# Optimization experiments

Measured on AMD Instinct MI355X. Metric: run time of the kernel, lower is better.

## Reference

```python
import jax, jax.numpy as jnp
import numpy as np

N_CLASSES = 3
FEAT_SIZES = (64, 32)  # source1 64x64, source2 32x32 for 512x512 input


def conv(x, w, b):
    # x: NCHW, w: OIHW, 3x3 SAME, stride 1
    y = jax.lax.conv_general_dilated(
        x, w, window_strides=(1, 1), padding='SAME',
        dimension_numbers=('NCHW', 'OIHW', 'NCHW'))
    return y + b[None, :, None, None]


def maxpool(x):
    return jax.lax.reduce_window(x, -jnp.inf, jax.lax.max,
                                 (1, 1, 2, 2), (1, 1, 2, 2), 'VALID')


def l2norm(x, gamma, eps=1e-10):
    # standard SSD L2Norm: per-position channel L2 normalize, learned per-channel scale
    n = jnp.sqrt(jnp.sum(x * x, axis=1, keepdims=True)) + eps
    return gamma[None, :, None, None] * x / n


def make_priors():
    # PriorBox: one prior per feature-map cell, normalized (cx, cy) centers
    ps = []
    for f in FEAT_SIZES:
        c = (jnp.arange(f, dtype=jnp.float32) + 0.5) / f
        cy, cx = jnp.meshgrid(c, c, indexing='ij')
        ps.append(jnp.stack([cx.ravel(), cy.ravel()], axis=1))  # [f*f, 2]
    return jnp.concatenate(ps, axis=0)  # [5120, 2]


def setup_inputs() -> dict:
    key = jax.random.key(0)
    ks = iter(jax.random.split(key, 32))

    def he(k, shape):
        fan_in = shape[1] * shape[2] * shape[3]
        return jax.random.normal(k, shape, jnp.float32) * (2.0 / fan_in) ** 0.5

    d = {'x': jax.random.normal(next(ks), (8, 2, 512, 512), jnp.float32)}
    shapes = [(64, 2, 3, 3), (64, 64, 3, 3), (128, 64, 3, 3), (128, 128, 3, 3),
              (256, 128, 3, 3), (256, 256, 3, 3), (256, 256, 3, 3), (256, 256, 3, 3)]
    for n, s in enumerate(shapes, 1):
        d[f'w{n}'] = he(next(ks), s)
        d[f'b{n}'] = jnp.zeros((s[0],), jnp.float32)
    d['g1'] = 20.0 * jnp.ones((256,), jnp.float32)  # L2Norm1 weight
    d['g2'] = 20.0 * jnp.ones((256,), jnp.float32)  # L2Norm2 weight
    for pre, oc in (('l', 2), ('c', N_CLASSES), ('r', 1)):
        for si in (1, 2):
            d[f'{pre}w{si}'] = he(next(ks), (oc, 256, 3, 3))
            d[f'{pre}b{si}'] = jnp.zeros((oc,), jnp.float32)
    return d


def reference(x, w1, b1, w2, b2, w3, b3, w4, b4, w5, b5, w6, b6, w7, b7, w8, b8,
              g1, g2, lw1, lb1, lw2, lb2, cw1, cb1, cw2, cb2, rw1, rb1, rw2, rb2):
    B = x.shape[0]
    r = jax.nn.relu
    # vgg[0:33]
    x = r(conv(x, w1, b1)); x = r(conv(x, w2, b2)); x = maxpool(x)
    x = r(conv(x, w3, b3)); x = r(conv(x, w4, b4)); x = maxpool(x)
    x = r(conv(x, w5, b5)); x = r(conv(x, w6, b6)); x = maxpool(x)
    s1 = l2norm(x, g1)                 # [B,256,64,64]
    # vgg[33:]
    x = maxpool(x)
    x = r(conv(x, w7, b7)); x = r(conv(x, w8, b8))
    s2 = l2norm(x, g2)                 # [B,256,32,32]

    def head(s, w_, b_):
        # conv -> permute(0,2,3,1) -> flatten, as in the torch forward
        return conv(s, w_, b_).transpose(0, 2, 3, 1).reshape(B, -1)

    loc = jnp.concatenate([head(s1, lw1, lb1), head(s2, lw2, lb2)], 1).reshape(B, -1, 2)
    conf = jnp.concatenate([head(s1, cw1, cb1), head(s2, cw2, cb2)], 1).reshape(B, -1, N_CLASSES)
    regr = jnp.concatenate([head(s1, rw1, rb1), head(s2, rw2, rb2)], 1).reshape(B, -1, 1)
    priors = make_priors()
    return loc, conf, regr, priors
```

## Files before the change

kernel.cpp:

```cpp
#include <hip/hip_runtime.h>

typedef _Float16 f16;
typedef _Float16 f16x8 __attribute__((ext_vector_type(8)));
typedef float f32x4 __attribute__((ext_vector_type(4)));

__device__ __forceinline__ f32x4 mfma16(f16x8 a, f16x8 b, f32x4 c) {
    return __builtin_amdgcn_mfma_f32_16x16x32_f16(a, b, c, 0, 0, 0);
}

template<int IC, int OC, int BX, int WY, int WO, int MT, bool POOL>
__global__ __launch_bounds__(256) void convmf_k(
    const f16* __restrict__ in, const f16* __restrict__ wt,
    const float* __restrict__ bias, f16* __restrict__ out,
    int H, int W, int ocBlocks, long inStride, long outStride)
{
    constexpr int WROWS = MT * 16 / BX;
    constexpr int BROWS = WROWS * WY;
    constexpr int SR = BROWS + 2;
    constexpr int SC = BX + 2;
    constexpr int LOG = (BX == 64) ? 6 : 5;
    static_assert(!POOL || (BX == 64 && MT == 8), "pool path assumes BX==64, MT==8");
    __shared__ f16 lds[SR * SC * 40];

    const int tid  = threadIdx.x;
    const int lane = tid & 63;
    const int wv   = tid >> 6;
    const int wy   = wv / WO;
    const int wo   = wv % WO;
    const int lm   = lane & 15;
    const int lk   = lane >> 4;
    const int x0   = blockIdx.x * BX;
    const int y0   = blockIdx.y * BROWS;
    const int zb   = blockIdx.z;
    const int n    = zb / ocBlocks;
    const int oc0  = (zb - n * ocBlocks) * (64 * WO) + wo * 64;
    in  += (long)n * inStride;
    out += (long)n * outStride;

    f32x4 acc[MT][4];
#pragma unroll
    for (int mt = 0; mt < MT; ++mt)
#pragma unroll
        for (int nt = 0; nt < 4; ++nt)
            acc[mt][nt] = (f32x4){0.f, 0.f, 0.f, 0.f};

    const int Wp = W + 2;
    for (int ic0 = 0; ic0 < IC; ic0 += 32) {
        if (ic0) __syncthreads();
        const f16* ip = in + ((long)y0 * Wp + x0) * IC + ic0;
        constexpr int TASKS = SR * SC * 4;
        for (int s = tid; s < TASKS; s += 256) {
            int r    = s / (SC * 4);
            int rem  = s - r * (SC * 4);
            int xcol = rem >> 2;
            int g    = rem & 3;
            f16x8 v = *(const f16x8*)(ip + ((long)r * Wp + xcol) * IC + g * 8);
            *(f16x8*)&lds[(r * SC + xcol) * 40 + g * 8] = v;
        }
        __syncthreads();

        for (int t = 0; t < 9; ++t) {
            int dy = t / 3, dx = t - dy * 3;
            const f16* wp = wt + ((long)t * OC + oc0) * IC + ic0 + lk * 8;
            f16x8 b0 = *(const f16x8*)(wp + (0 * 16 + lm) * IC);
            f16x8 b1 = *(const f16x8*)(wp + (1 * 16 + lm) * IC);
            f16x8 b2 = *(const f16x8*)(wp + (2 * 16 + lm) * IC);
            f16x8 b3 = *(const f16x8*)(wp + (3 * 16 + lm) * IC);
#pragma unroll
            for (int mt = 0; mt < MT; ++mt) {
                int pos = mt * 16 + lm;
                int xx = pos & (BX - 1);
                int yy = wy * WROWS + (pos >> LOG);
                f16x8 a = *(const f16x8*)&lds[((yy + dy) * SC + xx + dx) * 40 + lk * 8];
                acc[mt][0] = mfma16(a, b0, acc[mt][0]);
                acc[mt][1] = mfma16(a, b1, acc[mt][1]);
                acc[mt][2] = mfma16(a, b2, acc[mt][2]);
                acc[mt][3] = mfma16(a, b3, acc[mt][3]);
            }
        }
    }

    if constexpr (!POOL) {
#pragma unroll
        for (int nt = 0; nt < 4; ++nt) {
            int oc = oc0 + nt * 16 + lm;
            float bs = bias[oc];
#pragma unroll
            for (int mt = 0; mt < MT; ++mt) {
#pragma unroll
                for (int r = 0; r < 4; ++r) {
                    int pos = mt * 16 + lk * 4 + r;
                    int xx = pos & (BX - 1);
                    int yy = wy * WROWS + (pos >> LOG);
                    float v = fmaxf(acc[mt][nt][r] + bs, 0.f);
                    out[((long)(y0 + yy + 1) * (W + 2) + (x0 + xx + 1)) * OC + oc] = (f16)v;
                }
            }
        }
    } else {
        const int Wo = W >> 1;
#pragma unroll
        for (int nt = 0; nt < 4; ++nt) {
            int oc = oc0 + nt * 16 + lm;
            float bs = bias[oc];
#pragma unroll
            for (int mt = 0; mt < 4; ++mt) {
#pragma unroll
                for (int r = 0; r < 4; r += 2) {
                    float v = fmaxf(fmaxf(acc[mt][nt][r], acc[mt][nt][r + 1]),
                                    fmaxf(acc[mt + 4][nt][r], acc[mt + 4][nt][r + 1]));
                    v = fmaxf(v + bs, 0.f);
                    int pos = mt * 16 + lk * 4 + r;
                    int xo = pos >> 1;
                    out[((long)((y0 >> 1) + wy + 1) * (Wo + 2) + ((x0 >> 1) + xo + 1)) * OC + oc] = (f16)v;
                }
            }
        }
    }
}

__global__ __launch_bounds__(256) void conv12_k(
    const float* __restrict__ x,
    const f16* __restrict__ wt1,
    const float* __restrict__ b1,
    const f16* __restrict__ wt2,
    const float* __restrict__ b2,
    f16* __restrict__ p1, int itemBase, long outStride)
{
    __shared__ f16 ldsx[12 * 68 * 2];
    __shared__ f16 a1t[10 * 66 * 40];
    const int tid = threadIdx.x;
    const int lane = tid & 63;
    const int wv = tid >> 6;
    const int lm = lane & 15;
    const int lk = lane >> 4;
    const int x0 = blockIdx.x * 64;
    const int y0 = blockIdx.y * 8;
    const float* xb = x + (long)(itemBase + blockIdx.z) * 2 * 512 * 512;
    f16* out = p1 + (long)blockIdx.z * outStride;

    for (int s = tid; s < 12 * 68 * 2; s += 256) {
        int ch = s & 1;
        int v = s >> 1;
        int r = v / 68, c = v - r * 68;
        int gy = y0 + r - 2, gx = x0 + c - 2;
        f16 val = (f16)0.f;
        if ((unsigned)gy < 512u && (unsigned)gx < 512u)
            val = (f16)xb[((long)ch * 512 + gy) * 512 + gx];
        ldsx[s] = val;
    }
    __syncthreads();

    f32x4 acc[8][4];
#pragma unroll
    for (int mt = 0; mt < 8; ++mt)
#pragma unroll
        for (int nt = 0; nt < 4; ++nt)
            acc[mt][nt] = (f32x4){0.f, 0.f, 0.f, 0.f};

    for (int cc = 0; cc < 2; ++cc) {
        if (cc) __syncthreads();

        {
            float bs0 = b1[cc * 32 + lm];
            float bs1 = b1[cc * 32 + 16 + lm];
            f16x8 bf0 = *(const f16x8*)(wt1 + (cc * 32 + lm) * 32 + lk * 8);
            f16x8 bf1 = *(const f16x8*)(wt1 + (cc * 32 + 16 + lm) * 32 + lk * 8);
            const int t0 = wv * 11;
            const int tn = (wv == 3) ? 9 : 11;
            for (int ti = 0; ti < tn; ++ti) {
                const int tile = t0 + ti;
                const int pixA = tile * 16 + lm;
                int rA = (pixA * 993) >> 16;
                int cA = pixA - rA * 66;
                f16x8 af;
#pragma unroll
                for (int j = 0; j < 8; ++j) {
                    int k = lk * 8 + j;
                    f16 v = (f16)0.f;
                    if (k < 18) {
                        int t = k >> 1, ic = k & 1;
                        int dy = (t * 22) >> 6;
                        int dx = t - 3 * dy;
                        v = ldsx[((rA + dy) * 68 + (cA + dx)) * 2 + ic];
                    }
                    af[j] = v;
                }
                f32x4 c0 = (f32x4){0.f, 0.f, 0.f, 0.f};
                f32x4 c1 = (f32x4){0.f, 0.f, 0.f, 0.f};
                c0 = mfma16(af, bf0, c0);
                c1 = mfma16(af, bf1, c1);
#pragma unroll
                for (int rr = 0; rr < 4; ++rr) {
                    int pix = tile * 16 + lk * 4 + rr;
                    if (pix < 660) {
                        int rP = (pix * 993) >> 16;
                        int cP = pix - rP * 66;
                        bool valid = ((unsigned)(y0 + rP - 1) < 512u) &&
                                     ((unsigned)(x0 + cP - 1) < 512u);
                        float v0 = valid ? fmaxf(c0[rr] + bs0, 0.f) : 0.f;
                        float v1 = valid ? fmaxf(c1[rr] + bs1, 0.f) : 0.f;
                        a1t[pix * 40 + lm] = (f16)v0;
                        a1t[pix * 40 + 16 + lm] = (f16)v1;
                    }
                }
            }
        }
        __syncthreads();

        const int ic0 = cc * 32;
        for (int t = 0; t < 9; ++t) {
            int dy = t / 3, dx = t - dy * 3;
            const f16* wp = wt2 + ((long)t * 64) * 64 + ic0 + lk * 8;
            f16x8 b0 = *(const f16x8*)(wp + (0 * 16 + lm) * 64);
            f16x8 bb1 = *(const f16x8*)(wp + (1 * 16 + lm) * 64);
            f16x8 b2v = *(const f16x8*)(wp + (2 * 16 + lm) * 64);
            f16x8 b3 = *(const f16x8*)(wp + (3 * 16 + lm) * 64);
#pragma unroll
            for (int mt = 0; mt < 8; ++mt) {
                int pos = mt * 16 + lm;
                int xx = pos & 63;
                int yy = wv * 2 + (pos >> 6);
                f16x8 a = *(const f16x8*)&a1t[((yy + dy) * 66 + xx + dx) * 40 + lk * 8];
                acc[mt][0] = mfma16(a, b0, acc[mt][0]);
                acc[mt][1] = mfma16(a, bb1, acc[mt][1]);
                acc[mt][2] = mfma16(a, b2v, acc[mt][2]);
                acc[mt][3] = mfma16(a, b3, acc[mt][3]);
            }
        }
    }

#pragma unroll
    for (int nt = 0; nt < 4; ++nt) {
        int oc = nt * 16 + lm;
        float bs = b2[oc];
#pragma unroll
        for (int mt = 0; mt < 4; ++mt) {
#pragma unroll
            for (int r = 0; r < 4; r += 2) {
                float v = fmaxf(fmaxf(acc[mt][nt][r], acc[mt][nt][r + 1]),
                                fmaxf(acc[mt + 4][nt][r], acc[mt + 4][nt][r + 1]));
                v = fmaxf(v + bs, 0.f);
                int pos = mt * 16 + lk * 4 + r;
                int xo = pos >> 1;
                out[((long)((y0 >> 1) + wv + 1) * 258 + ((x0 >> 1) + xo + 1)) * 64 + oc] = (f16)v;
            }
        }
    }
}

template<int BX>
__global__ __launch_bounds__(256) void headconv_k(
    const f16* __restrict__ s, long sStride, const f16* __restrict__ wth,
    const float* __restrict__ lb, const float* __restrict__ cb, const float* __restrict__ rb,
    float* __restrict__ loc, float* __restrict__ conf, float* __restrict__ regr,
    int W, int posoff)
{
    constexpr int BY = (BX == 64) ? 1 : 2;
    constexpr int SR = BY + 2, SC = BX + 2;
    constexpr int LOG = (BX == 64) ? 6 : 5;
    __shared__ f16 lds[SR * SC * 40];
    const int tid = threadIdx.x;
    const int lane = tid & 63;
    const int wv = tid >> 6;
    const int lm = lane & 15;
    const int lk = lane >> 4;
    const int y0 = blockIdx.y * BY;
    const int b = blockIdx.z;
    s += (long)b * sStride;

    f32x4 acc = (f32x4){0.f, 0.f, 0.f, 0.f};
    const int Wp = W + 2;
    for (int ic0 = 0; ic0 < 256; ic0 += 32) {
        if (ic0) __syncthreads();
        const f16* ip = s + (long)y0 * Wp * 256 + ic0;
        constexpr int TASKS = SR * SC * 4;
        for (int t = tid; t < TASKS; t += 256) {
            int r = t / (SC * 4);
            int rem = t - r * (SC * 4);
            int xcol = rem >> 2, g = rem & 3;
            f16x8 v = *(const f16x8*)(ip + ((long)r * Wp + xcol) * 256 + g * 8);
            *(f16x8*)&lds[(r * SC + xcol) * 40 + g * 8] = v;
        }
        __syncthreads();
        for (int t = 0; t < 9; ++t) {
            int dy = t / 3, dx = t - dy * 3;
            f16x8 bf = *(const f16x8*)(wth + ((long)t * 16 + lm) * 256 + ic0 + lk * 8);
            int pos = wv * 16 + lm;
            int xx = pos & (BX - 1), yy = pos >> LOG;
            f16x8 a = *(const f16x8*)&lds[((yy + dy) * SC + xx + dx) * 40 + lk * 8];
            acc = mfma16(a, bf, acc);
        }
    }
#pragma unroll
    for (int r = 0; r < 4; ++r) {
        int pos = wv * 16 + lk * 4 + r;
        int xx = pos & (BX - 1), yy = pos >> LOG;
        int P = posoff + (y0 + yy) * W + xx;
        float v = acc[r];
        if (lm < 2)       loc[((long)b * 5120 + P) * 2 + lm]       = v + lb[lm];
        else if (lm < 5)  conf[((long)b * 5120 + P) * 3 + (lm - 2)] = v + cb[lm - 2];
        else if (lm == 5) regr[(long)b * 5120 + P]                  = v + rb[0];
    }
}

__global__ __launch_bounds__(256) void cvt_wt_k(const float* __restrict__ w, f16* __restrict__ wt,
                                                int OC, int IC)
{
    int idx = blockIdx.x * 256 + threadIdx.x;
    if (idx >= OC * IC) return;
    int oc = idx / IC, ic = idx - oc * IC;
#pragma unroll
    for (int t = 0; t < 9; ++t)
        wt[((long)t * OC + oc) * IC + ic] = (f16)w[(long)idx * 9 + t];
}

__global__ __launch_bounds__(64) void cvt_wt1_k(const float* __restrict__ w, f16* __restrict__ wt1)
{
    int oc = threadIdx.x;
#pragma unroll
    for (int k = 0; k < 32; ++k) {
        f16 v = (f16)0.f;
        if (k < 18) {
            int t = k >> 1, ic = k & 1;
            v = (f16)w[((long)oc * 2 + ic) * 9 + t];
        }
        wt1[oc * 32 + k] = v;
    }
}

__global__ __launch_bounds__(256) void cvt_wth_k(const float* __restrict__ lw, const float* __restrict__ cw,
                                                 const float* __restrict__ rw, f16* __restrict__ wth)
{
    int idx = blockIdx.x * 256 + threadIdx.x;
    if (idx >= 9 * 16 * 256) return;
    int t = idx / (16 * 256);
    int r = (idx / 256) & 15;
    int ic = idx & 255;
    float v = 0.f;
    if (r < 2)      v = lw[((long)r * 256 + ic) * 9 + t];
    else if (r < 5) v = cw[((long)(r - 2) * 256 + ic) * 9 + t];
    else if (r == 5) v = rw[(long)ic * 9 + t];
    wth[((long)t * 16 + r) * 256 + ic] = (f16)v;
}

__global__ __launch_bounds__(256) void halo_k(f16* __restrict__ buf, int W, int H, int C,
                                              long stride, int items)
{
    int per = (2 * (W + 2) + 2 * H) * C;
    long total = (long)per * items;
    long idx = (long)blockIdx.x * 256 + threadIdx.x;
    if (idx >= total) return;
    int n = idx / per;
    int j = idx - (long)n * per;
    int c = j % C, p = j / C;
    int row, col;
    if (p < W + 2) { row = 0; col = p; }
    else if (p < 2 * (W + 2)) { row = H + 1; col = p - (W + 2); }
    else { int q = p - 2 * (W + 2); row = 1 + (q >> 1); col = (q & 1) ? (W + 1) : 0; }
    buf[(long)n * stride + ((long)row * (W + 2) + col) * C + c] = (f16)0.f;
}

__global__ __launch_bounds__(256) void l2n_k(const f16* __restrict__ in, const float* __restrict__ g,
                                             f16* __restrict__ out, int W, long stride, int total)
{
    int i = blockIdx.x * 256 + threadIdx.x;
    if (i >= total) return;
    int b = i / (W * W);
    int rem = i - b * W * W;
    int y = rem / W, x = rem - y * W;
    long off = (long)b * stride + ((long)(y + 1) * (W + 2) + x + 1) * 256;
    const f16* p = in + off;
    f16* q = out + off;
    float s = 0.f;
    for (int gg = 0; gg < 32; ++gg) {
        f16x8 v = *(const f16x8*)(p + gg * 8);
#pragma unroll
        for (int j = 0; j < 8; ++j) { float f = (float)v[j]; s = fmaf(f, f, s); }
    }
    float inv = 1.f / (sqrtf(s) + 1e-10f);
    for (int gg = 0; gg < 32; ++gg) {
        f16x8 v = *(const f16x8*)(p + gg * 8);
        f16x8 o;
#pragma unroll
        for (int j = 0; j < 8; ++j) o[j] = (f16)(g[gg * 8 + j] * ((float)v[j] * inv));
        *(f16x8*)(q + gg * 8) = o;
    }
}

__global__ __launch_bounds__(256) void mp_k(const f16* __restrict__ in, f16* __restrict__ out)
{
    int idx = blockIdx.x * 256 + threadIdx.x;
    if (idx >= 8 * 32 * 32 * 32) return;
    int gg = idx & 31;
    int xo = (idx >> 5) & 31;
    int yo = (idx >> 10) & 31;
    int b = idx >> 15;
    const f16* p = in + (long)b * 1115136 + ((long)(2 * yo + 1) * 66 + 2 * xo + 1) * 256 + gg * 8;
    f16x8 a0 = *(const f16x8*)p;
    f16x8 a1 = *(const f16x8*)(p + 256);
    f16x8 a2 = *(const f16x8*)(p + 66 * 256);
    f16x8 a3 = *(const f16x8*)(p + 66 * 256 + 256);
    f16x8 o;
#pragma unroll
    for (int j = 0; j < 8; ++j)
        o[j] = (f16)fmaxf(fmaxf((float)a0[j], (float)a1[j]), fmaxf((float)a2[j], (float)a3[j]));
    *(f16x8*)(out + (long)b * 295936 + ((long)(yo + 1) * 34 + xo + 1) * 256 + gg * 8) = o;
}

__global__ __launch_bounds__(256) void priors_k(float* __restrict__ out)
{
    int r = blockIdx.x * 256 + threadIdx.x;
    if (r >= 5120) return;
    float cx, cy;
    if (r < 4096) {
        int i = r >> 6, j = r & 63;
        cx = (j + 0.5f) / 64.0f; cy = (i + 0.5f) / 64.0f;
    } else {
        int rr = r - 4096;
        int i = rr >> 5, j = rr & 31;
        cx = (j + 0.5f) / 32.0f; cy = (i + 0.5f) / 32.0f;
    }
    out[2 * r] = cx;
    out[2 * r + 1] = cy;
}

extern "C" void kernel_launch(void* const* d_in, const int* in_sizes, int n_in,
                              void* d_out, int out_size, void* d_ws, size_t ws_size,
                              hipStream_t stream)
{
    const float* x  = (const float*)d_in[0];
    const float* w1 = (const float*)d_in[1];  const float* b1 = (const float*)d_in[2];
    const float* w2 = (const float*)d_in[3];  const float* b2 = (const float*)d_in[4];
    const float* w3 = (const float*)d_in[5];  const float* b3 = (const float*)d_in[6];
    const float* w4 = (const float*)d_in[7];  const float* b4 = (const float*)d_in[8];
    const float* w5 = (const float*)d_in[9];  const float* b5 = (const float*)d_in[10];
    const float* w6 = (const float*)d_in[11]; const float* b6 = (const float*)d_in[12];
    const float* w7 = (const float*)d_in[13]; const float* b7 = (const float*)d_in[14];
    const float* w8 = (const float*)d_in[15]; const float* b8 = (const float*)d_in[16];
    const float* g1 = (const float*)d_in[17]; const float* g2 = (const float*)d_in[18];
    const float* lw1 = (const float*)d_in[19]; const float* lb1 = (const float*)d_in[20];
    const float* lw2 = (const float*)d_in[21]; const float* lb2 = (const float*)d_in[22];
    const float* cw1 = (const float*)d_in[23]; const float* cb1 = (const float*)d_in[24];
    const float* cw2 = (const float*)d_in[25]; const float* cb2 = (const float*)d_in[26];
    const float* rw1 = (const float*)d_in[27]; const float* rb1 = (const float*)d_in[28];
    const float* rw2 = (const float*)d_in[29]; const float* rb2 = (const float*)d_in[30];

    f16* wsh = (f16*)d_ws;
    f16* wt2  = wsh + 0;
    f16* wt3  = wsh + 36864;
    f16* wt4  = wsh + 110592;
    f16* wt5  = wsh + 258048;
    f16* wt6  = wsh + 552960;
    f16* wt7  = wsh + 1142784;
    f16* wt8  = wsh + 1732608;
    f16* wt1  = wsh + 2322432;
    f16* wth1 = wsh + 2324480;
    f16* wth2 = wsh + 2361344;
    f16* x6p  = wsh + 2398208;
    const long PI = 11319296;

    const long R1S = 4260096;
    const long PS  = 12780288;
    const long PH2 = 18391040;

    int G = 1;
    for (int g = 8; g >= 1; g >>= 1) {
        long ext = (long)g * PS; if (ext < PH2) ext = PH2;
        if (2.0 * (double)(PI + ext) <= (double)ws_size) { G = g; break; }
    }
    const int NGRP = 8 / G;

    f16* p1 = wsh + PI;
    f16* a3 = wsh + PI + R1S;
    f16* p2 = p1;
    f16* a5 = a3;
    f16* s1 = wsh + PI;
    f16* p4 = wsh + PI + 8921088;
    f16* a7 = wsh + PI + 11288576;
    f16* a8 = wsh + PI + 13656064;
    f16* s2 = wsh + PI + 16023552;

    float* loc  = (float*)d_out;
    float* conf = loc + 81920;
    float* regr = loc + 204800;
    float* pri  = loc + 245760;

    cvt_wt_k<<<dim3((64 * 64 + 255) / 256), 256, 0, stream>>>(w2, wt2, 64, 64);
    cvt_wt_k<<<dim3((128 * 64 + 255) / 256), 256, 0, stream>>>(w3, wt3, 128, 64);
    cvt_wt_k<<<dim3((128 * 128 + 255) / 256), 256, 0, stream>>>(w4, wt4, 128, 128);
    cvt_wt_k<<<dim3((256 * 128 + 255) / 256), 256, 0, stream>>>(w5, wt5, 256, 128);
    cvt_wt_k<<<dim3((256 * 256 + 255) / 256), 256, 0, stream>>>(w6, wt6, 256, 256);
    cvt_wt_k<<<dim3((256 * 256 + 255) / 256), 256, 0, stream>>>(w7, wt7, 256, 256);
    cvt_wt_k<<<dim3((256 * 256 + 255) / 256), 256, 0, stream>>>(w8, wt8, 256, 256);
    cvt_wt1_k<<<dim3(1), 64, 0, stream>>>(w1, wt1);
    cvt_wth_k<<<dim3(144), 256, 0, stream>>>(lw1, cw1, rw1, wth1);
    cvt_wth_k<<<dim3(144), 256, 0, stream>>>(lw2, cw2, rw2, wth2);

    for (int grp = 0; grp < NGRP; ++grp) {
        f16* x6g = x6p + (long)grp * G * 1115136;
        halo_k<<<dim3((G * (2 * 258 + 2 * 256) * 64 + 255) / 256), 256, 0, stream>>>(p1, 256, 256, 64, PS, G);
        halo_k<<<dim3((G * (2 * 258 + 2 * 256) * 128 + 255) / 256), 256, 0, stream>>>(a3, 256, 256, 128, PS, G);
        conv12_k<<<dim3(8, 64, G), 256, 0, stream>>>(x, wt1, b1, wt2, b2, p1, grp * G, PS);
        convmf_k<64, 128, 64, 2, 2, 8, false><<<dim3(4, 64, G), 256, 0, stream>>>(
            p1, wt3, b3, a3, 256, 256, 1, PS, PS);
        halo_k<<<dim3((G * (2 * 130 + 2 * 128) * 128 + 255) / 256), 256, 0, stream>>>(p2, 128, 128, 128, PS, G);
        convmf_k<128, 128, 64, 2, 2, 8, true><<<dim3(4, 64, G), 256, 0, stream>>>(
            a3, wt4, b4, p2, 256, 256, 1, PS, PS);
        halo_k<<<dim3((G * (2 * 130 + 2 * 128) * 256 + 255) / 256), 256, 0, stream>>>(a5, 128, 128, 256, PS, G);
        convmf_k<128, 256, 64, 2, 2, 8, false><<<dim3(2, 32, 2 * G), 256, 0, stream>>>(
            p2, wt5, b5, a5, 128, 128, 2, PS, PS);
        convmf_k<256, 256, 64, 2, 2, 8, true><<<dim3(2, 32, 2 * G), 256, 0, stream>>>(
            a5, wt6, b6, x6g, 128, 128, 2, PS, 1115136);
    }

    halo_k<<<dim3((8 * (2 * 66 + 2 * 64) * 256 + 255) / 256), 256, 0, stream>>>(s1, 64, 64, 256, 1115136, 8);
    halo_k<<<dim3((8 * (2 * 34 + 2 * 32) * 256 + 255) / 256), 256, 0, stream>>>(p4, 32, 32, 256, 295936, 8);
    halo_k<<<dim3((8 * (2 * 34 + 2 * 32) * 256 + 255) / 256), 256, 0, stream>>>(a7, 32, 32, 256, 295936, 8);
    halo_k<<<dim3((8 * (2 * 34 + 2 * 32) * 256 + 255) / 256), 256, 0, stream>>>(s2, 32, 32, 256, 295936, 8);

    l2n_k<<<dim3((32768 + 255) / 256), 256, 0, stream>>>(x6p, g1, s1, 64, 1115136, 32768);
    mp_k<<<dim3((262144 + 255) / 256), 256, 0, stream>>>(x6p, p4);
    convmf_k<256, 256, 32, 2, 2, 4, false><<<dim3(1, 8, 16), 256, 0, stream>>>(
        p4, wt7, b7, a7, 32, 32, 2, 295936, 295936);
    convmf_k<256, 256, 32, 2, 2, 4, false><<<dim3(1, 8, 16), 256, 0, stream>>>(
        a7, wt8, b8, a8, 32, 32, 2, 295936, 295936);
    l2n_k<<<dim3((8192 + 255) / 256), 256, 0, stream>>>(a8, g2, s2, 32, 295936, 8192);

    headconv_k<64><<<dim3(1, 64, 8), 256, 0, stream>>>(
        s1, 1115136, wth1, lb1, cb1, rb1, loc, conf, regr, 64, 0);
    headconv_k<32><<<dim3(1, 16, 8), 256, 0, stream>>>(
        s2, 295936, wth2, lb2, cb2, rb2, loc, conf, regr, 32, 4096);
    priors_k<<<dim3(20), 256, 0, stream>>>(pri);

    (void)in_sizes; (void)n_in; (void)out_size; (void)ws_size;
}
```

Measured before the change: 1.351 ms.

## Halve per-wave output-channel tile and raise occupancy in conv kernels

Adds an NT template parameter so each wave computes 32 output channels instead of 64 in the large-resolution conv layers, doubling the grid's oc-block count, and sets launch_bounds(256,4) to target more resident blocks. conv12_k is also restructured to a 4-row tile with waves split over rows and output channels, shrinking LDS and accumulator registers. The aim is higher occupancy and better latency hiding, but each input tile is now loaded and reused across fewer output channels, which raises LDS fill and global input traffic.

```diff
diff --git a/kernel.cpp b/kernel.cpp
--- a/kernel.cpp
+++ b/kernel.cpp
@@ -8,8 +8,8 @@
     return __builtin_amdgcn_mfma_f32_16x16x32_f16(a, b, c, 0, 0, 0);
 }
 
-template<int IC, int OC, int BX, int WY, int WO, int MT, bool POOL>
-__global__ __launch_bounds__(256) void convmf_k(
+template<int IC, int OC, int BX, int WY, int WO, int MT, int NT, bool POOL>
+__global__ __launch_bounds__(256, 4) void convmf_k(
     const f16* __restrict__ in, const f16* __restrict__ wt,
     const float* __restrict__ bias, f16* __restrict__ out,
     int H, int W, int ocBlocks, long inStride, long outStride)
@@ -33,15 +33,15 @@
     const int y0   = blockIdx.y * BROWS;
     const int zb   = blockIdx.z;
     const int n    = zb / ocBlocks;
-    const int oc0  = (zb - n * ocBlocks) * (64 * WO) + wo * 64;
+    const int oc0  = (zb - n * ocBlocks) * (16 * NT * WO) + wo * (16 * NT);
     in  += (long)n * inStride;
     out += (long)n * outStride;
 
-    f32x4 acc[MT][4];
+    f32x4 acc[MT][NT];
 #pragma unroll
     for (int mt = 0; mt < MT; ++mt)
 #pragma unroll
-        for (int nt = 0; nt < 4; ++nt)
+        for (int nt = 0; nt < NT; ++nt)
             acc[mt][nt] = (f32x4){0.f, 0.f, 0.f, 0.f};
 
     const int Wp = W + 2;
@@ -62,27 +62,26 @@
         for (int t = 0; t < 9; ++t) {
             int dy = t / 3, dx = t - dy * 3;
             const f16* wp = wt + ((long)t * OC + oc0) * IC + ic0 + lk * 8;
-            f16x8 b0 = *(const f16x8*)(wp + (0 * 16 + lm) * IC);
-            f16x8 b1 = *(const f16x8*)(wp + (1 * 16 + lm) * IC);
-            f16x8 b2 = *(const f16x8*)(wp + (2 * 16 + lm) * IC);
-            f16x8 b3 = *(const f16x8*)(wp + (3 * 16 + lm) * IC);
+            f16x8 bfr[NT];
+#pragma unroll
+            for (int nt = 0; nt < NT; ++nt)
+                bfr[nt] = *(const f16x8*)(wp + (nt * 16 + lm) * IC);
 #pragma unroll
             for (int mt = 0; mt < MT; ++mt) {
                 int pos = mt * 16 + lm;
                 int xx = pos & (BX - 1);
                 int yy = wy * WROWS + (pos >> LOG);
                 f16x8 a = *(const f16x8*)&lds[((yy + dy) * SC + xx + dx) * 40 + lk * 8];
-                acc[mt][0] = mfma16(a, b0, acc[mt][0]);
-                acc[mt][1] = mfma16(a, b1, acc[mt][1]);
-                acc[mt][2] = mfma16(a, b2, acc[mt][2]);
-                acc[mt][3] = mfma16(a, b3, acc[mt][3]);
+#pragma unroll
+                for (int nt = 0; nt < NT; ++nt)
+                    acc[mt][nt] = mfma16(a, bfr[nt], acc[mt][nt]);
             }
         }
     }
 
     if constexpr (!POOL) {
 #pragma unroll
-        for (int nt = 0; nt < 4; ++nt) {
+        for (int nt = 0; nt < NT; ++nt) {
             int oc = oc0 + nt * 16 + lm;
             float bs = bias[oc];
 #pragma unroll
@@ -100,7 +99,7 @@
     } else {
         const int Wo = W >> 1;
 #pragma unroll
-        for (int nt = 0; nt < 4; ++nt) {
+        for (int nt = 0; nt < NT; ++nt) {
             int oc = oc0 + nt * 16 + lm;
             float bs = bias[oc];
 #pragma unroll
@@ -119,7 +118,7 @@
     }
 }
 
-__global__ __launch_bounds__(256) void conv12_k(
+__global__ __launch_bounds__(256, 4) void conv12_k(
     const float* __restrict__ x,
     const f16* __restrict__ wt1,
     const float* __restrict__ b1,
@@ -127,19 +126,21 @@
     const float* __restrict__ b2,
     f16* __restrict__ p1, int itemBase, long outStride)
 {
-    __shared__ f16 ldsx[12 * 68 * 2];
-    __shared__ f16 a1t[10 * 66 * 40];
+    __shared__ f16 ldsx[8 * 68 * 2];
+    __shared__ f16 a1t[6 * 66 * 40];
     const int tid = threadIdx.x;
     const int lane = tid & 63;
     const int wv = tid >> 6;
+    const int wy = wv >> 1;
+    const int wo = wv & 1;
     const int lm = lane & 15;
     const int lk = lane >> 4;
     const int x0 = blockIdx.x * 64;
-    const int y0 = blockIdx.y * 8;
+    const int y0 = blockIdx.y * 4;
     const float* xb = x + (long)(itemBase + blockIdx.z) * 2 * 512 * 512;
     f16* out = p1 + (long)blockIdx.z * outStride;
 
-    for (int s = tid; s < 12 * 68 * 2; s += 256) {
+    for (int s = tid; s < 8 * 68 * 2; s += 256) {
         int ch = s & 1;
         int v = s >> 1;
         int r = v / 68, c = v - r * 68;
@@ -151,11 +152,11 @@
     }
     __syncthreads();
 
-    f32x4 acc[8][4];
+    f32x4 acc[8][2];
 #pragma unroll
     for (int mt = 0; mt < 8; ++mt)
 #pragma unroll
-        for (int nt = 0; nt < 4; ++nt)
+        for (int nt = 0; nt < 2; ++nt)
             acc[mt][nt] = (f32x4){0.f, 0.f, 0.f, 0.f};
 
     for (int cc = 0; cc < 2; ++cc) {
@@ -166,13 +167,11 @@
             float bs1 = b1[cc * 32 + 16 + lm];
             f16x8 bf0 = *(const f16x8*)(wt1 + (cc * 32 + lm) * 32 + lk * 8);
             f16x8 bf1 = *(const f16x8*)(wt1 + (cc * 32 + 16 + lm) * 32 + lk * 8);
-            const int t0 = wv * 11;
-            const int tn = (wv == 3) ? 9 : 11;
-            for (int ti = 0; ti < tn; ++ti) {
-                const int tile = t0 + ti;
+            for (int tile = wv; tile < 25; tile += 4) {
                 const int pixA = tile * 16 + lm;
-                int rA = (pixA * 993) >> 16;
-                int cA = pixA - rA * 66;
+                const int pixg = (pixA < 396) ? pixA : 0;
+                int rA = (pixg * 993) >> 16;
+                int cA = pixg - rA * 66;
                 f16x8 af;
 #pragma unroll
                 for (int j = 0; j < 8; ++j) {
@@ -193,7 +192,7 @@
 #pragma unroll
                 for (int rr = 0; rr < 4; ++rr) {
                     int pix = tile * 16 + lk * 4 + rr;
-                    if (pix < 660) {
+                    if (pix < 396) {
                         int rP = (pix * 993) >> 16;
                         int cP = pix - rP * 66;
                         bool valid = ((unsigned)(y0 + rP - 1) < 512u) &&
@@ -211,28 +210,24 @@
         const int ic0 = cc * 32;
         for (int t = 0; t < 9; ++t) {
             int dy = t / 3, dx = t - dy * 3;
-            const f16* wp = wt2 + ((long)t * 64) * 64 + ic0 + lk * 8;
-            f16x8 b0 = *(const f16x8*)(wp + (0 * 16 + lm) * 64);
+            const f16* wp = wt2 + ((long)t * 64 + wo * 32) * 64 + ic0 + lk * 8;
+            f16x8 bb0 = *(const f16x8*)(wp + (0 * 16 + lm) * 64);
             f16x8 bb1 = *(const f16x8*)(wp + (1 * 16 + lm) * 64);
-            f16x8 b2v = *(const f16x8*)(wp + (2 * 16 + lm) * 64);
-            f16x8 b3 = *(const f16x8*)(wp + (3 * 16 + lm) * 64);
 #pragma unroll
             for (int mt = 0; mt < 8; ++mt) {
                 int pos = mt * 16 + lm;
                 int xx = pos & 63;
-                int yy = wv * 2 + (pos >> 6);
+                int yy = wy * 2 + (pos >> 6);
                 f16x8 a = *(const f16x8*)&a1t[((yy + dy) * 66 + xx + dx) * 40 + lk * 8];
-                acc[mt][0] = mfma16(a, b0, acc[mt][0]);
+                acc[mt][0] = mfma16(a, bb0, acc[mt][0]);
                 acc[mt][1] = mfma16(a, bb1, acc[mt][1]);
-                acc[mt][2] = mfma16(a, b2v, acc[mt][2]);
-                acc[mt][3] = mfma16(a, b3, acc[mt][3]);
             }
         }
     }
 
 #pragma unroll
-    for (int nt = 0; nt < 4; ++nt) {
-        int oc = nt * 16 + lm;
+    for (int nt = 0; nt < 2; ++nt) {
+        int oc = wo * 32 + nt * 16 + lm;
         float bs = b2[oc];
 #pragma unroll
         for (int mt = 0; mt < 4; ++mt) {
@@ -243,7 +238,7 @@
                 v = fmaxf(v + bs, 0.f);
                 int pos = mt * 16 + lk * 4 + r;
                 int xo = pos >> 1;
-                out[((long)((y0 >> 1) + wv + 1) * 258 + ((x0 >> 1) + xo + 1)) * 64 + oc] = (f16)v;
+                out[((long)((y0 >> 1) + wy + 1) * 258 + ((x0 >> 1) + xo + 1)) * 64 + oc] = (f16)v;
             }
         }
     }
@@ -501,17 +496,17 @@
         f16* x6g = x6p + (long)grp * G * 1115136;
         halo_k<<<dim3((G * (2 * 258 + 2 * 256) * 64 + 255) / 256), 256, 0, stream>>>(p1, 256, 256, 64, PS, G);
         halo_k<<<dim3((G * (2 * 258 + 2 * 256) * 128 + 255) / 256), 256, 0, stream>>>(a3, 256, 256, 128, PS, G);
-        conv12_k<<<dim3(8, 64, G), 256, 0, stream>>>(x, wt1, b1, wt2, b2, p1, grp * G, PS);
-        convmf_k<64, 128, 64, 2, 2, 8, false><<<dim3(4, 64, G), 256, 0, stream>>>(
-            p1, wt3, b3, a3, 256, 256, 1, PS, PS);
+        conv12_k<<<dim3(8, 128, G), 256, 0, stream>>>(x, wt1, b1, wt2, b2, p1, grp * G, PS);
+        convmf_k<64, 128, 64, 2, 2, 8, 2, false><<<dim3(4, 64, 2 * G), 256, 0, stream>>>(
+            p1, wt3, b3, a3, 256, 256, 2, PS, PS);
         halo_k<<<dim3((G * (2 * 130 + 2 * 128) * 128 + 255) / 256), 256, 0, stream>>>(p2, 128, 128, 128, PS, G);
-        convmf_k<128, 128, 64, 2, 2, 8, true><<<dim3(4, 64, G), 256, 0, stream>>>(
-            a3, wt4, b4, p2, 256, 256, 1, PS, PS);
+        convmf_k<128, 128, 64, 2, 2, 8, 2, true><<<dim3(4, 64, 2 * G), 256, 0, stream>>>(
+            a3, wt4, b4, p2, 256, 256, 2, PS, PS);
         halo_k<<<dim3((G * (2 * 130 + 2 * 128) * 256 + 255) / 256), 256, 0, stream>>>(a5, 128, 128, 256, PS, G);
-        convmf_k<128, 256, 64, 2, 2, 8, false><<<dim3(2, 32, 2 * G), 256, 0, stream>>>(
-            p2, wt5, b5, a5, 128, 128, 2, PS, PS);
-        convmf_k<256, 256, 64, 2, 2, 8, true><<<dim3(2, 32, 2 * G), 256, 0, stream>>>(
-            a5, wt6, b6, x6g, 128, 128, 2, PS, 1115136);
+        convmf_k<128, 256, 64, 2, 2, 8, 2, false><<<dim3(2, 32, 4 * G), 256, 0, stream>>>(
+            p2, wt5, b5, a5, 128, 128, 4, PS, PS);
+        convmf_k<256, 256, 64, 2, 2, 8, 2, true><<<dim3(2, 32, 4 * G), 256, 0, stream>>>(
+            a5, wt6, b6, x6g, 128, 128, 4, PS, 1115136);
     }
 
     halo_k<<<dim3((8 * (2 * 66 + 2 * 64) * 256 + 255) / 256), 256, 0, stream>>>(s1, 64, 64, 256, 1115136, 8);
@@ -521,9 +516,9 @@
 
     l2n_k<<<dim3((32768 + 255) / 256), 256, 0, stream>>>(x6p, g1, s1, 64, 1115136, 32768);
     mp_k<<<dim3((262144 + 255) / 256), 256, 0, stream>>>(x6p, p4);
-    convmf_k<256, 256, 32, 2, 2, 4, false><<<dim3(1, 8, 16), 256, 0, stream>>>(
+    convmf_k<256, 256, 32, 2, 2, 4, 4, false><<<dim3(1, 8, 16), 256, 0, stream>>>(
         p4, wt7, b7, a7, 32, 32, 2, 295936, 295936);
-    convmf_k<256, 256, 32, 2, 2, 4, false><<<dim3(1, 8, 16), 256, 0, stream>>>(
+    convmf_k<256, 256, 32, 2, 2, 4, 4, false><<<dim3(1, 8, 16), 256, 0, stream>>>(
         a7, wt8, b8, a8, 32, 32, 2, 295936, 295936);
     l2n_k<<<dim3((8192 + 255) / 256), 256, 0, stream>>>(a8, g2, s2, 32, 295936, 8192);
 
```

After: 2.228 ms. 64.9% more time.

## Halve conv12 block height and split output channels across wave pairs

Applied to the files above, without the earlier changes.

The fused conv1+conv2+pool kernel now handles 4 input rows per block instead of 8. Waves are arranged 2x2, with each pair splitting the 64 output channels. This cuts LDS use (smaller ldsx and a1t tiles) and accumulator registers per thread, which should allow more blocks per CU and doubles the grid. The conv1 A-fragment gather now reads both input channels with one 32-bit LDS load instead of per-element 16-bit loads. In exchange, the halo recompute ratio for conv1 rises, since each block recomputes 6 rows of conv1 for 4 output rows.

```diff
diff --git a/kernel.cpp b/kernel.cpp
--- a/kernel.cpp
+++ b/kernel.cpp
@@ -127,19 +127,21 @@
     const float* __restrict__ b2,
     f16* __restrict__ p1, int itemBase, long outStride)
 {
-    __shared__ f16 ldsx[12 * 68 * 2];
-    __shared__ f16 a1t[10 * 66 * 40];
+    __shared__ f16 ldsx[8 * 68 * 2];
+    __shared__ f16 a1t[6 * 66 * 40];
     const int tid = threadIdx.x;
     const int lane = tid & 63;
     const int wv = tid >> 6;
+    const int wy = wv >> 1;
+    const int wo = wv & 1;
     const int lm = lane & 15;
     const int lk = lane >> 4;
     const int x0 = blockIdx.x * 64;
-    const int y0 = blockIdx.y * 8;
+    const int y0 = blockIdx.y * 4;
     const float* xb = x + (long)(itemBase + blockIdx.z) * 2 * 512 * 512;
     f16* out = p1 + (long)blockIdx.z * outStride;
 
-    for (int s = tid; s < 12 * 68 * 2; s += 256) {
+    for (int s = tid; s < 8 * 68 * 2; s += 256) {
         int ch = s & 1;
         int v = s >> 1;
         int r = v / 68, c = v - r * 68;
@@ -151,11 +153,11 @@
     }
     __syncthreads();
 
-    f32x4 acc[8][4];
+    f32x4 acc[8][2];
 #pragma unroll
     for (int mt = 0; mt < 8; ++mt)
 #pragma unroll
-        for (int nt = 0; nt < 4; ++nt)
+        for (int nt = 0; nt < 2; ++nt)
             acc[mt][nt] = (f32x4){0.f, 0.f, 0.f, 0.f};
 
     for (int cc = 0; cc < 2; ++cc) {
@@ -166,34 +168,31 @@
             float bs1 = b1[cc * 32 + 16 + lm];
             f16x8 bf0 = *(const f16x8*)(wt1 + (cc * 32 + lm) * 32 + lk * 8);
             f16x8 bf1 = *(const f16x8*)(wt1 + (cc * 32 + 16 + lm) * 32 + lk * 8);
-            const int t0 = wv * 11;
-            const int tn = (wv == 3) ? 9 : 11;
-            for (int ti = 0; ti < tn; ++ti) {
-                const int tile = t0 + ti;
+            for (int tile = wv; tile < 25; tile += 4) {
                 const int pixA = tile * 16 + lm;
-                int rA = (pixA * 993) >> 16;
-                int cA = pixA - rA * 66;
-                f16x8 af;
-#pragma unroll
-                for (int j = 0; j < 8; ++j) {
-                    int k = lk * 8 + j;
-                    f16 v = (f16)0.f;
-                    if (k < 18) {
-                        int t = k >> 1, ic = k & 1;
+                const int pixg = (pixA < 396) ? pixA : 0;
+                int rA = (pixg * 993) >> 16;
+                int cA = pixg - rA * 66;
+                union { f16x8 v; unsigned u[4]; } af;
+#pragma unroll
+                for (int jj = 0; jj < 4; ++jj) {
+                    int t = lk * 4 + jj;
+                    unsigned uv = 0u;
+                    if (t < 9) {
                         int dy = (t * 22) >> 6;
                         int dx = t - 3 * dy;
-                        v = ldsx[((rA + dy) * 68 + (cA + dx)) * 2 + ic];
+                        uv = *(const unsigned*)&ldsx[((rA + dy) * 68 + (cA + dx)) * 2];
                     }
-                    af[j] = v;
+                    af.u[jj] = uv;
                 }
                 f32x4 c0 = (f32x4){0.f, 0.f, 0.f, 0.f};
                 f32x4 c1 = (f32x4){0.f, 0.f, 0.f, 0.f};
-                c0 = mfma16(af, bf0, c0);
-                c1 = mfma16(af, bf1, c1);
+                c0 = mfma16(af.v, bf0, c0);
+                c1 = mfma16(af.v, bf1, c1);
 #pragma unroll
                 for (int rr = 0; rr < 4; ++rr) {
                     int pix = tile * 16 + lk * 4 + rr;
-                    if (pix < 660) {
+                    if (pix < 396) {
                         int rP = (pix * 993) >> 16;
                         int cP = pix - rP * 66;
                         bool valid = ((unsigned)(y0 + rP - 1) < 512u) &&
@@ -211,28 +210,24 @@
         const int ic0 = cc * 32;
         for (int t = 0; t < 9; ++t) {
             int dy = t / 3, dx = t - dy * 3;
-            const f16* wp = wt2 + ((long)t * 64) * 64 + ic0 + lk * 8;
-            f16x8 b0 = *(const f16x8*)(wp + (0 * 16 + lm) * 64);
+            const f16* wp = wt2 + ((long)t * 64 + wo * 32) * 64 + ic0 + lk * 8;
+            f16x8 bb0 = *(const f16x8*)(wp + (0 * 16 + lm) * 64);
             f16x8 bb1 = *(const f16x8*)(wp + (1 * 16 + lm) * 64);
-            f16x8 b2v = *(const f16x8*)(wp + (2 * 16 + lm) * 64);
-            f16x8 b3 = *(const f16x8*)(wp + (3 * 16 + lm) * 64);
 #pragma unroll
             for (int mt = 0; mt < 8; ++mt) {
                 int pos = mt * 16 + lm;
                 int xx = pos & 63;
-                int yy = wv * 2 + (pos >> 6);
+                int yy = wy * 2 + (pos >> 6);
                 f16x8 a = *(const f16x8*)&a1t[((yy + dy) * 66 + xx + dx) * 40 + lk * 8];
-                acc[mt][0] = mfma16(a, b0, acc[mt][0]);
+                acc[mt][0] = mfma16(a, bb0, acc[mt][0]);
                 acc[mt][1] = mfma16(a, bb1, acc[mt][1]);
-                acc[mt][2] = mfma16(a, b2v, acc[mt][2]);
-                acc[mt][3] = mfma16(a, b3, acc[mt][3]);
             }
         }
     }
 
 #pragma unroll
-    for (int nt = 0; nt < 4; ++nt) {
-        int oc = nt * 16 + lm;
+    for (int nt = 0; nt < 2; ++nt) {
+        int oc = wo * 32 + nt * 16 + lm;
         float bs = b2[oc];
 #pragma unroll
         for (int mt = 0; mt < 4; ++mt) {
@@ -243,7 +238,7 @@
                 v = fmaxf(v + bs, 0.f);
                 int pos = mt * 16 + lk * 4 + r;
                 int xo = pos >> 1;
-                out[((long)((y0 >> 1) + wv + 1) * 258 + ((x0 >> 1) + xo + 1)) * 64 + oc] = (f16)v;
+                out[((long)((y0 >> 1) + wy + 1) * 258 + ((x0 >> 1) + xo + 1)) * 64 + oc] = (f16)v;
             }
         }
     }
@@ -501,7 +496,7 @@
         f16* x6g = x6p + (long)grp * G * 1115136;
         halo_k<<<dim3((G * (2 * 258 + 2 * 256) * 64 + 255) / 256), 256, 0, stream>>>(p1, 256, 256, 64, PS, G);
         halo_k<<<dim3((G * (2 * 258 + 2 * 256) * 128 + 255) / 256), 256, 0, stream>>>(a3, 256, 256, 128, PS, G);
-        conv12_k<<<dim3(8, 64, G), 256, 0, stream>>>(x, wt1, b1, wt2, b2, p1, grp * G, PS);
+        conv12_k<<<dim3(8, 128, G), 256, 0, stream>>>(x, wt1, b1, wt2, b2, p1, grp * G, PS);
         convmf_k<64, 128, 64, 2, 2, 8, false><<<dim3(4, 64, G), 256, 0, stream>>>(
             p1, wt3, b3, a3, 256, 256, 1, PS, PS);
         halo_k<<<dim3((G * (2 * 130 + 2 * 128) * 128 + 255) / 256), 256, 0, stream>>>(p2, 128, 128, 128, PS, G);
```

After: 1.419 ms. 5.0% more time.
